# Kernel tuning notes

Hardware: AMD Instinct MI355X
Metric: run time of the kernel (lower is better)

The kernel has to match this reference:

```python
import jax, jax.numpy as jnp
import numpy as np

B, Q, K, H = 32, 256, 256, 128

def setup_inputs() -> dict:
    key = jax.random.key(0)
    k1, k2, k3, k4 = jax.random.split(key, 4)
    queries = jax.random.normal(k1, (B, Q, H), dtype=jnp.float32)
    keys = jax.random.normal(k2, (B, K, H), dtype=jnp.float32)
    values = jax.random.normal(k3, (B, K, H), dtype=jnp.float32)
    # nn.Linear(hidden_size, 1, bias=False) weight, stored as a length-H vector
    w = jax.random.normal(k4, (H,), dtype=jnp.float32) * (1.0 / np.sqrt(H))
    return {"queries": queries, "keys": keys, "values": values, "w": w}


def reference(queries, keys, values, w):
    # Y: [B, Q, K, H] broadcast sum, then tanh
    Y = jnp.tanh(queries[:, :, None, :] + keys[:, None, :, :])
    # scores: [B, Q, K] = Y @ w
    scores = jnp.einsum("bqkh,h->bqk", Y, w)
    attn = jax.nn.softmax(scores, axis=-1)
    # output: [B, Q, Hv]
    return jnp.einsum("bqk,bkv->bqv", attn, values)
```

## Files before the change

### kernel.cpp

```cpp
#include <hip/hip_runtime.h>
#include <math.h>

#define C2 2.8853900817779268f

typedef __attribute__((address_space(3))) unsigned int       lds_u32;
typedef const __attribute__((address_space(1))) unsigned int g_u32;

__device__ __forceinline__ void stage16(const float* g, float* l) {
    __builtin_amdgcn_global_load_lds((g_u32*)g, (lds_u32*)l, 16, 0, 0);
}

__global__ __launch_bounds__(512) void addattn_kernel(
    const float* __restrict__ q_g, const float* __restrict__ k_g,
    const float* __restrict__ v_g, const float* __restrict__ w_g,
    float* __restrict__ out)
{
    __shared__ float kbuf[32768];
    __shared__ float sB[8192];

    const int tid  = threadIdx.x;
    const int lane = tid & 63;
    const int wv   = __builtin_amdgcn_readfirstlane(tid >> 6);

    const int xcd = blockIdx.x & 7;
    const int sub = blockIdx.x >> 3;
    const int b   = (xcd << 2) + (sub >> 3);
    const int qr0 = ((sub & 7) << 5) + (wv << 2);

    float* strip = sB + (wv << 10);

    if (lane < 32) *(float4*)&strip[512 + (lane << 2)] = ((const float4*)w_g)[lane];
    {
        const float* qb = q_g + (size_t)(b * 256 + qr0) * 128;
        #pragma unroll
        for (int j = 0; j < 2; ++j) {
            int f = lane + (j << 6);
            int r = f >> 5, c = f & 31;
            float4 qv = *(const float4*)(qb + (r << 7) + (c << 2));
            float4 E;
            E.x = __builtin_amdgcn_exp2f(C2 * qv.x);
            E.y = __builtin_amdgcn_exp2f(C2 * qv.y);
            E.z = __builtin_amdgcn_exp2f(C2 * qv.z);
            E.w = __builtin_amdgcn_exp2f(C2 * qv.w);
            *(float4*)&strip[(r << 7) + (c << 2)] = E;
        }
    }

    {
        const float4* kg4 = (const float4*)(k_g + (size_t)b * 32768);
        #pragma unroll
        for (int j = 0; j < 16; ++j) {
            int f = tid + (j << 9);
            float4 kv = kg4[f];
            int k = f >> 5, g = f & 31;
            float4 E;
            E.x = __builtin_amdgcn_exp2f(C2 * kv.x);
            E.y = __builtin_amdgcn_exp2f(C2 * kv.y);
            E.z = __builtin_amdgcn_exp2f(C2 * kv.z);
            E.w = __builtin_amdgcn_exp2f(C2 * kv.w);
            int rot = ((k & 63) + g) & 63;
            *(float4*)&kbuf[((k >> 6) << 13) + (g << 8) + (rot << 2)] = E;
        }
    }
    __syncthreads();

    float s[4][4];
    #pragma unroll
    for (int t = 0; t < 4; ++t)
        #pragma unroll
        for (int r = 0; r < 4; ++r) s[t][r] = 0.f;

    #pragma unroll 4
    for (int g = 0; g < 32; ++g) {
        float4 w4 = *(const float4*)&strip[512 + (g << 2)];
        float4 e0 = *(const float4*)&strip[g << 2];
        float4 e1 = *(const float4*)&strip[128 + (g << 2)];
        float4 e2 = *(const float4*)&strip[256 + (g << 2)];
        float4 e3 = *(const float4*)&strip[384 + (g << 2)];
        const int rot = (((lane + g) & 63) << 2) + (g << 8);
        #pragma unroll
        for (int t = 0; t < 4; ++t) {
            float4 k4 = *(const float4*)&kbuf[(t << 13) + rot];
            #define RB(E, S)                                                   \
            {                                                                  \
                float d0 = fmaf(E.x, k4.x, 1.f), d1 = fmaf(E.y, k4.y, 1.f);    \
                float d2 = fmaf(E.z, k4.z, 1.f), d3 = fmaf(E.w, k4.w, 1.f);    \
                float P01 = d0 * d1, P23 = d2 * d3;                            \
                float N01 = fmaf(w4.x, d1, w4.y * d0);                         \
                float N23 = fmaf(w4.z, d3, w4.w * d2);                         \
                float num = fmaf(N01, P23, N23 * P01);                         \
                S = fmaf(num, __builtin_amdgcn_rcpf(P01 * P23), S);            \
            }
            RB(e0, s[t][0])
            RB(e1, s[t][1])
            RB(e2, s[t][2])
            RB(e3, s[t][3])
            #undef RB
        }
    }

    #pragma unroll
    for (int r = 0; r < 4; ++r) {
        float p0 = __builtin_amdgcn_exp2f(-C2 * s[0][r]);
        float p1 = __builtin_amdgcn_exp2f(-C2 * s[1][r]);
        float p2 = __builtin_amdgcn_exp2f(-C2 * s[2][r]);
        float p3 = __builtin_amdgcn_exp2f(-C2 * s[3][r]);
        float sum = (p0 + p1) + (p2 + p3);
        #pragma unroll
        for (int off = 32; off; off >>= 1) sum += __shfl_xor(sum, off);
        float inv = __builtin_amdgcn_rcpf(sum);
        strip[(r << 8) + lane]       = p0 * inv;
        strip[(r << 8) + 64 + lane]  = p1 * inv;
        strip[(r << 8) + 128 + lane] = p2 * inv;
        strip[(r << 8) + 192 + lane] = p3 * inv;
    }

    __syncthreads();

    {
        const float* vb = v_g + (size_t)b * 32768;
        #pragma unroll
        for (int c = 0; c < 16; ++c) {
            int chunk = (wv << 4) + c;
            stage16(vb + (chunk << 8) + (lane << 2), kbuf + (chunk << 8));
        }
    }
    __syncthreads();

    float2 o0, o1, o2, o3;
    o0.x = o0.y = o1.x = o1.y = 0.f;
    o2.x = o2.y = o3.x = o3.y = 0.f;
    #pragma unroll 4
    for (int j4 = 0; j4 < 64; ++j4) {
        float4 a0 = *(const float4*)(strip + (j4 << 2));
        float4 a1 = *(const float4*)(strip + 256 + (j4 << 2));
        float4 a2 = *(const float4*)(strip + 512 + (j4 << 2));
        float4 a3 = *(const float4*)(strip + 768 + (j4 << 2));
        #pragma unroll
        for (int i = 0; i < 4; ++i) {
            float2 v2 = *(const float2*)&kbuf[(((j4 << 2) + i) << 7) + (lane << 1)];
            float c0 = (&a0.x)[i], c1 = (&a1.x)[i], c2 = (&a2.x)[i], c3 = (&a3.x)[i];
            o0.x = fmaf(c0, v2.x, o0.x); o0.y = fmaf(c0, v2.y, o0.y);
            o1.x = fmaf(c1, v2.x, o1.x); o1.y = fmaf(c1, v2.y, o1.y);
            o2.x = fmaf(c2, v2.x, o2.x); o2.y = fmaf(c2, v2.y, o2.y);
            o3.x = fmaf(c3, v2.x, o3.x); o3.y = fmaf(c3, v2.y, o3.y);
        }
    }

    float* ob = out + (size_t)(b * 256 + qr0) * 128 + (lane << 1);
    *(float2*)(ob)       = o0;
    *(float2*)(ob + 128) = o1;
    *(float2*)(ob + 256) = o2;
    *(float2*)(ob + 384) = o3;
}

extern "C" void kernel_launch(void* const* d_in, const int* in_sizes, int n_in,
                              void* d_out, int out_size, void* d_ws, size_t ws_size,
                              hipStream_t stream) {
    const float* q = (const float*)d_in[0];
    const float* k = (const float*)d_in[1];
    const float* v = (const float*)d_in[2];
    const float* w = (const float*)d_in[3];
    float* out = (float*)d_out;
    addattn_kernel<<<256, 512, 0, stream>>>(q, k, v, w, out);
}
```

Baseline: 43.17 us.

## Split fused kernel into score kernel over key halves and separate PV kernel

Splits the single fused kernel in two. The first kernel computes scores with each block covering half of the keys, which doubles the grid to 512 blocks and halves the LDS footprint so more blocks can be resident. It writes log2-scaled scores to workspace. The second kernel does the softmax and the P·V product. This trades extra global traffic for the 8 MB score buffer, plus a second launch, for more parallelism in the heavy tanh-score phase.

```diff
diff --git a/kernel.cpp b/kernel.cpp
--- a/kernel.cpp
+++ b/kernel.cpp
@@ -10,13 +10,12 @@
     __builtin_amdgcn_global_load_lds((g_u32*)g, (lds_u32*)l, 16, 0, 0);
 }
 
-__global__ __launch_bounds__(512) void addattn_kernel(
+__global__ __launch_bounds__(512, 4) void score_kernel(
     const float* __restrict__ q_g, const float* __restrict__ k_g,
-    const float* __restrict__ v_g, const float* __restrict__ w_g,
-    float* __restrict__ out)
+    const float* __restrict__ w_g, float* __restrict__ sc_ws)
 {
-    __shared__ float kbuf[32768];
-    __shared__ float sB[8192];
+    __shared__ float kbuf[16384];
+    __shared__ float sEq[4096];
 
     const int tid  = threadIdx.x;
     const int lane = tid & 63;
@@ -24,12 +23,14 @@
 
     const int xcd = blockIdx.x & 7;
     const int sub = blockIdx.x >> 3;
-    const int b   = (xcd << 2) + (sub >> 3);
-    const int qr0 = ((sub & 7) << 5) + (wv << 2);
+    const int b   = (xcd << 2) + (sub >> 4);
+    const int rem = sub & 15;
+    const int kh  = rem >> 3;
+    const int rg  = rem & 7;
+    const int qr0 = (rg << 5) + (wv << 2);
 
-    float* strip = sB + (wv << 10);
+    float* strip = sEq + (wv << 9);
 
-    if (lane < 32) *(float4*)&strip[512 + (lane << 2)] = ((const float4*)w_g)[lane];
     {
         const float* qb = q_g + (size_t)(b * 256 + qr0) * 128;
         #pragma unroll
@@ -47,9 +48,9 @@
     }
 
     {
-        const float4* kg4 = (const float4*)(k_g + (size_t)b * 32768);
+        const float4* kg4 = (const float4*)(k_g + (size_t)b * 32768 + (kh << 14));
         #pragma unroll
-        for (int j = 0; j < 16; ++j) {
+        for (int j = 0; j < 8; ++j) {
             int f = tid + (j << 9);
             float4 kv = kg4[f];
             int k = f >> 5, g = f & 31;
@@ -64,22 +65,22 @@
     }
     __syncthreads();
 
-    float s[4][4];
+    float s[2][4];
     #pragma unroll
-    for (int t = 0; t < 4; ++t)
+    for (int t = 0; t < 2; ++t)
         #pragma unroll
         for (int r = 0; r < 4; ++r) s[t][r] = 0.f;
 
     #pragma unroll 4
     for (int g = 0; g < 32; ++g) {
-        float4 w4 = *(const float4*)&strip[512 + (g << 2)];
+        float4 w4 = *(const float4*)(w_g + (g << 2));
         float4 e0 = *(const float4*)&strip[g << 2];
         float4 e1 = *(const float4*)&strip[128 + (g << 2)];
         float4 e2 = *(const float4*)&strip[256 + (g << 2)];
         float4 e3 = *(const float4*)&strip[384 + (g << 2)];
         const int rot = (((lane + g) & 63) << 2) + (g << 8);
         #pragma unroll
-        for (int t = 0; t < 4; ++t) {
+        for (int t = 0; t < 2; ++t) {
             float4 k4 = *(const float4*)&kbuf[(t << 13) + rot];
             #define RB(E, S)                                                   \
             {                                                                  \
@@ -101,21 +102,29 @@
 
     #pragma unroll
     for (int r = 0; r < 4; ++r) {
-        float p0 = __builtin_amdgcn_exp2f(-C2 * s[0][r]);
-        float p1 = __builtin_amdgcn_exp2f(-C2 * s[1][r]);
-        float p2 = __builtin_amdgcn_exp2f(-C2 * s[2][r]);
-        float p3 = __builtin_amdgcn_exp2f(-C2 * s[3][r]);
-        float sum = (p0 + p1) + (p2 + p3);
-        #pragma unroll
-        for (int off = 32; off; off >>= 1) sum += __shfl_xor(sum, off);
-        float inv = __builtin_amdgcn_rcpf(sum);
-        strip[(r << 8) + lane]       = p0 * inv;
-        strip[(r << 8) + 64 + lane]  = p1 * inv;
-        strip[(r << 8) + 128 + lane] = p2 * inv;
-        strip[(r << 8) + 192 + lane] = p3 * inv;
+        float* br = sc_ws + (size_t)(b * 256 + qr0 + r) * 256 + (kh << 7) + lane;
+        br[0]  = -C2 * s[0][r];
+        br[64] = -C2 * s[1][r];
     }
+}
 
-    __syncthreads();
+__global__ __launch_bounds__(512) void pv_kernel(
+    const float* __restrict__ sc_ws, const float* __restrict__ v_g,
+    float* __restrict__ out)
+{
+    __shared__ float kbuf[32768];
+    __shared__ float sB[8192];
+
+    const int tid  = threadIdx.x;
+    const int lane = tid & 63;
+    const int wv   = __builtin_amdgcn_readfirstlane(tid >> 6);
+
+    const int xcd = blockIdx.x & 7;
+    const int sub = blockIdx.x >> 3;
+    const int b   = (xcd << 2) + (sub >> 3);
+    const int qr0 = ((sub & 7) << 5) + (wv << 2);
+
+    float* strip = sB + (wv << 10);
 
     {
         const float* vb = v_g + (size_t)b * 32768;
@@ -124,6 +133,22 @@
             int chunk = (wv << 4) + c;
             stage16(vb + (chunk << 8) + (lane << 2), kbuf + (chunk << 8));
         }
+    }
+
+    #pragma unroll
+    for (int r = 0; r < 4; ++r) {
+        const float* srow = sc_ws + (size_t)(b * 256 + qr0 + r) * 256;
+        float4 sv = *(const float4*)(srow + (lane << 2));
+        float p0 = __builtin_amdgcn_exp2f(sv.x);
+        float p1 = __builtin_amdgcn_exp2f(sv.y);
+        float p2 = __builtin_amdgcn_exp2f(sv.z);
+        float p3 = __builtin_amdgcn_exp2f(sv.w);
+        float sum = (p0 + p1) + (p2 + p3);
+        #pragma unroll
+        for (int off = 32; off; off >>= 1) sum += __shfl_xor(sum, off);
+        float inv = __builtin_amdgcn_rcpf(sum);
+        float4 at; at.x = p0 * inv; at.y = p1 * inv; at.z = p2 * inv; at.w = p3 * inv;
+        *(float4*)&strip[(r << 8) + (lane << 2)] = at;
     }
     __syncthreads();
 
@@ -162,5 +187,7 @@
     const float* v = (const float*)d_in[2];
     const float* w = (const float*)d_in[3];
     float* out = (float*)d_out;
-    addattn_kernel<<<256, 512, 0, stream>>>(q, k, v, w, out);
+    float* sc  = (float*)d_ws;
+    score_kernel<<<512, 512, 0, stream>>>(q, k, w, sc);
+    pv_kernel<<<256, 512, 0, stream>>>(sc, v, out);
 }
```

After: 44.39 us. +2.8%, slower.
